# Optimization experiments

Measured on AMD Instinct MI355X. Metric: run time of the kernel, lower is better.

The kernel has to match this reference:

```python
import jax, jax.numpy as jnp
import numpy as np

N = 100000      # nodes
E = 1600000     # edges (avg degree 16)
F_IN = 128      # num_node_features (embedding vocab)
H = 32          # hidden_channels
C = 16          # num_classes
G = 64          # graphs in batch
NEG_SLOPE = 0.2  # GATConv default LeakyReLU slope


def setup_inputs() -> dict:
    key = jax.random.key(0)
    ks = jax.random.split(key, 12)
    x = jax.random.normal(ks[0], (N, F_IN), dtype=jnp.float32)
    edge_index = jax.random.randint(ks[1], (2, E), 0, N)
    batch = jnp.sort(jax.random.randint(ks[2], (N,), 0, G))
    s = 1.0 / np.sqrt(H).astype(np.float32)
    emb = jax.random.normal(ks[3], (F_IN, H), dtype=jnp.float32) * s
    W1 = jax.random.normal(ks[4], (H, H), dtype=jnp.float32) * s
    a1_src = jax.random.normal(ks[5], (H,), dtype=jnp.float32) * s
    a1_dst = jax.random.normal(ks[6], (H,), dtype=jnp.float32) * s
    b1 = jnp.zeros((H,), dtype=jnp.float32)
    W2 = jax.random.normal(ks[7], (H, C), dtype=jnp.float32) * s
    a2_src = jax.random.normal(ks[8], (C,), dtype=jnp.float32) * (1.0 / np.sqrt(C).astype(np.float32))
    a2_dst = jax.random.normal(ks[9], (C,), dtype=jnp.float32) * (1.0 / np.sqrt(C).astype(np.float32))
    b2 = jnp.zeros((C,), dtype=jnp.float32)
    return {"x": x, "edge_index": edge_index, "batch": batch,
            "emb": emb, "W1": W1, "a1_src": a1_src, "a1_dst": a1_dst, "b1": b1,
            "W2": W2, "a2_src": a2_src, "a2_dst": a2_dst, "b2": b2}


def gat_conv(h_in, src, dst, W, a_src, a_dst, bias):
    # h: [N, D]; per-edge attention alpha(e) = softmax_dst(leaky_relu(as[src]+ad[dst]))
    h = h_in @ W                                  # [N, D_out]
    al_s = h @ a_src                              # [N]
    al_d = h @ a_dst                              # [N]
    e = al_s[src] + al_d[dst]                     # [E]
    e = jnp.where(e > 0, e, NEG_SLOPE * e)        # leaky_relu
    m = jax.ops.segment_max(e, dst, num_segments=N)
    ex = jnp.exp(e - m[dst])
    denom = jax.ops.segment_sum(ex, dst, num_segments=N)
    alpha = ex / (denom[dst] + 1e-16)             # [E]
    out = jax.ops.segment_sum(alpha[:, None] * h[src], dst, num_segments=N)
    return out + bias


def reference(x, edge_index, batch, emb, W1, a1_src, a1_dst, b1, W2, a2_src, a2_dst, b2):
    # embedding lookup via argmax over feature dim
    idx = jnp.argmax(x, axis=1)                   # [N]
    h = emb[idx]                                  # [N, H]
    # add self loops (GATConv default)
    loops = jnp.arange(N, dtype=edge_index.dtype)
    src = jnp.concatenate([edge_index[0], loops])
    dst = jnp.concatenate([edge_index[1], loops])
    h = gat_conv(h, src, dst, W1, a1_src, a1_dst, b1)
    h = jax.nn.relu(h)
    # dropout is identity in eval mode
    h = gat_conv(h, src, dst, W2, a2_src, a2_dst, b2)   # [N, C]
    # global mean pool over graphs
    sums = jax.ops.segment_sum(h, batch, num_segments=G)         # [G, C]
    cnts = jax.ops.segment_sum(jnp.ones((N,), h.dtype), batch, num_segments=G)
    pooled = sums / jnp.maximum(cnts, 1.0)[:, None]
    return jax.nn.softmax(pooled, axis=1)
```

## Files before the change

kernel.cpp:

```cpp
#include <hip/hip_runtime.h>
#include <hip/hip_fp16.h>
#include <cmath>

#define HDIM 32
#define CDIM 16
#define FDIM 128
#define GDIM 64
#define NEG 0.2f
#define NN 100000
#define PPART 1024
#define CAPP 2048
#define WMAX 98
#define KA_BLOCKS 128

__device__ __forceinline__ float leaky(float e) { return e > 0.f ? e : NEG * e; }

__device__ __forceinline__ int part_of(int d) {
  return (int)(((unsigned)d << 10) / (unsigned)NN);
}
__device__ __forceinline__ int base_of(int p) {
  return (p * NN + (PPART - 1)) >> 10;
}

__global__ void k0_precompute(const float* __restrict__ emb, const float* __restrict__ W1,
                              const float* __restrict__ a1s, const float* __restrict__ a1d,
                              float* __restrict__ h1p, float* __restrict__ als1p,
                              float* __restrict__ ald1p) {
  __shared__ float sW1[HDIM * HDIM];
  int t = threadIdx.x;
  for (int i = t; i < HDIM * HDIM; i += 128) sW1[i] = W1[i];
  __syncthreads();
  int v = t;
  float hrow[HDIM];
#pragma unroll
  for (int k = 0; k < HDIM; ++k) hrow[k] = 0.f;
  for (int j = 0; j < HDIM; ++j) {
    float e = emb[v * HDIM + j];
#pragma unroll
    for (int k = 0; k < HDIM; ++k) hrow[k] += e * sW1[j * HDIM + k];
  }
  float s = 0.f, d = 0.f;
  for (int k = 0; k < HDIM; ++k) {
    h1p[v * HDIM + k] = hrow[k];
    s += hrow[k] * a1s[k];
    d += hrow[k] * a1d[k];
  }
  als1p[v] = s;
  ald1p[v] = d;
}

__global__ __launch_bounds__(256) void k1_argmax(const float* __restrict__ x,
                                                 int* __restrict__ idx, int N) {
  int wid = (blockIdx.x * blockDim.x + threadIdx.x) >> 6;
  int lane = threadIdx.x & 63;
  if (wid >= N) return;
  const float2* xr = (const float2*)(x + (size_t)wid * FDIM);
  float2 f = xr[lane];
  float best;
  int bi;
  if (f.y > f.x) { best = f.y; bi = 2 * lane + 1; } else { best = f.x; bi = 2 * lane; }
#pragma unroll
  for (int off = 32; off >= 1; off >>= 1) {
    float ov = __shfl_xor(best, off);
    int oi = __shfl_xor(bi, off);
    if (ov > best || (ov == best && oi < bi)) { best = ov; bi = oi; }
  }
  if (lane == 0) idx[wid] = bi;
}

__global__ __launch_bounds__(512) void kA_partition(const int* __restrict__ src,
                                                    const int* __restrict__ dst,
                                                    const int* __restrict__ idx,
                                                    int* __restrict__ pcnt,
                                                    unsigned* __restrict__ pay, int E) {
  __shared__ int lcount[PPART];
  __shared__ int gbase[PPART];
  int t = threadIdx.x;
  for (int i = t; i < PPART; i += 512) lcount[i] = 0;
  __syncthreads();
  int per = (E + KA_BLOCKS - 1) / KA_BLOCKS;
  int e0 = blockIdx.x * per, e1 = min(e0 + per, E);
  for (int e = e0 + t; e < e1; e += 512) atomicAdd(&lcount[part_of(dst[e])], 1);
  __syncthreads();
  for (int i = t; i < PPART; i += 512) gbase[i] = atomicAdd(&pcnt[i * 16], lcount[i]);
  __syncthreads();
  for (int e = e0 + t; e < e1; e += 512) {
    int d = dst[e], s = src[e];
    int p = part_of(d);
    int dloc = d - base_of(p);
    int pos = atomicAdd(&gbase[p], 1);
    if (pos < CAPP)
      pay[(size_t)p * CAPP + pos] =
          ((unsigned)dloc << 24) | ((unsigned)idx[s] << 17) | (unsigned)s;
  }
}

__global__ __launch_bounds__(512) void kB_layer1(const int* __restrict__ pcnt,
                                                 const unsigned* __restrict__ pay,
                                                 const int* __restrict__ idx,
                                                 const float* __restrict__ h1p,
                                                 const float* __restrict__ als1p,
                                                 const float* __restrict__ ald1p,
                                                 const float* __restrict__ b1,
                                                 const float* __restrict__ W2,
                                                 const float* __restrict__ a2s,
                                                 const float* __restrict__ a2d,
                                                 unsigned* __restrict__ pay2,
                                                 int* __restrict__ rpg,
                                                 __half2* __restrict__ h2h,
                                                 float* __restrict__ als2,
                                                 float* __restrict__ ald2, int N) {
  __shared__ float sh1p[FDIM * HDIM];
  __shared__ unsigned spay[CAPP];
  __shared__ int shist[WMAX];
  __shared__ int srp[WMAX + 1];
  __shared__ int soff[WMAX];
  __shared__ float sals1p[FDIM];
  __shared__ float sald1w[WMAX];
  __shared__ int sidxw[WMAX];
  __shared__ float sW2[HDIM * CDIM];
  __shared__ float sb1[HDIM];
  __shared__ float sa2s[CDIM], sa2d[CDIM];
  __shared__ float sstage[512];
  int t = threadIdx.x;
  int p = blockIdx.x;
  int base = base_of(p);
  int wend = base_of(p + 1); if (wend > N) wend = N;
  int wlen = wend - base;
  for (int i = t; i < FDIM * HDIM; i += 512) sh1p[i] = h1p[i];
  for (int i = t; i < HDIM * CDIM; i += 512) sW2[i] = W2[i];
  if (t < FDIM) sals1p[t] = als1p[t];
  if (t < HDIM) sb1[t] = b1[t];
  if (t < CDIM) { sa2s[t] = a2s[t]; sa2d[t] = a2d[t]; }
  if (t < WMAX) shist[t] = 0;
  for (int i = t; i < wlen; i += 512) {
    int ii = idx[base + i];
    sidxw[i] = ii;
    sald1w[i] = ald1p[ii];
  }
  __syncthreads();
  int cnt = min(pcnt[p * 16], CAPP);
  const unsigned* pm = pay + (size_t)p * CAPP;
  unsigned pwreg[4];
#pragma unroll
  for (int k = 0; k < 4; ++k) {
    int i = t + k * 512;
    if (i < cnt) {
      unsigned pw = pm[i];
      pwreg[k] = pw;
      atomicAdd(&shist[pw >> 24], 1);
    }
  }
  __syncthreads();
  if (t < 64) {
    int l = t;
    int v0 = (l < WMAX) ? shist[l] : 0;
    int v1 = (64 + l < WMAX) ? shist[64 + l] : 0;
    int s0 = v0, s1 = v1;
#pragma unroll
    for (int o = 1; o < 64; o <<= 1) {
      int u0 = __shfl_up(s0, o);
      int u1 = __shfl_up(s1, o);
      if (l >= o) { s0 += u0; s1 += u1; }
    }
    int tot0 = __shfl(s0, 63);
    if (l < WMAX) { srp[l] = s0 - v0; soff[l] = s0 - v0; }
    int i1 = 64 + l;
    if (i1 <= WMAX) {
      int ex = tot0 + s1 - v1;
      srp[i1] = ex;
      if (i1 < WMAX) soff[i1] = ex;
    }
  }
  __syncthreads();
#pragma unroll
  for (int k = 0; k < 4; ++k) {
    int i = t + k * 512;
    if (i < cnt) {
      unsigned pw = pwreg[k];
      int slot = atomicAdd(&soff[pw >> 24], 1);
      spay[slot] = pw;
    }
  }
  __syncthreads();
  for (int i = t; i < cnt; i += 512) pay2[(size_t)p * CAPP + i] = spay[i];
  for (int i = t; i <= wlen; i += 512) rpg[p * (WMAX + 1) + i] = srp[i];
  int g = t >> 5, c = t & 31;
  int j = c & 15, h = c >> 4;
  for (int i = g; i < wlen; i += 16) {
    int r0 = srp[i], r1 = srp[i + 1];
    float aldi = sald1w[i];
    float acc = 0.f, den = 0.f;
    for (int r = r0; r < r1; ++r) {
      unsigned pw = spay[r];
      int ivs = (pw >> 17) & 127;
      float w = __expf(leaky(sals1p[ivs] + aldi));
      acc += w * sh1p[ivs * HDIM + c];
      den += w;
    }
    int iv = sidxw[i];
    float wself = __expf(leaky(sals1p[iv] + aldi));
    acc += wself * sh1p[iv * HDIM + c];
    den += wself;
    float hr = fmaxf(acc / (den + 1e-16f) + sb1[c], 0.f);
    sstage[g * 32 + c] = hr;
    float pj = 0.f;
#pragma unroll
    for (int q = 0; q < 16; ++q) {
      int cc = h * 16 + q;
      pj += sstage[g * 32 + cc] * sW2[cc * CDIM + j];
    }
    pj += __shfl_xor(pj, 16);
    int n = base + i;
    float pjo = __shfl_xor(pj, 1);
    if (c < CDIM && !(c & 1))
      h2h[(size_t)n * 8 + (c >> 1)] = __floats2half2_rn(pj, pjo);
    float us = pj * sa2s[j], ud = pj * sa2d[j];
    us += __shfl_xor(us, 8); us += __shfl_xor(us, 4);
    us += __shfl_xor(us, 2); us += __shfl_xor(us, 1);
    ud += __shfl_xor(ud, 8); ud += __shfl_xor(ud, 4);
    ud += __shfl_xor(ud, 2); ud += __shfl_xor(ud, 1);
    if (c == 0) { als2[n] = us; ald2[n] = ud; }
  }
}

__global__ __launch_bounds__(512) void kC_layer2(const int* __restrict__ rpg,
                                                 const unsigned* __restrict__ pay2,
                                                 const float* __restrict__ als2,
                                                 const float* __restrict__ ald2,
                                                 const __half2* __restrict__ h2h,
                                                 const float* __restrict__ b2,
                                                 const int* __restrict__ batch,
                                                 float* __restrict__ pooled,
                                                 int* __restrict__ cnts, int N) {
  __shared__ int srp[WMAX + 1];
  __shared__ float sald2w[WMAX];
  __shared__ float sals2w[WMAX];
  __shared__ int sbatchw[WMAX];
  __shared__ float pl[GDIM * CDIM];
  __shared__ int cl[GDIM];
  __shared__ float sb2[CDIM];
  int t = threadIdx.x;
  int p = blockIdx.x;
  int base = base_of(p);
  int wend = base_of(p + 1); if (wend > N) wend = N;
  int wlen = wend - base;
  for (int i = t; i < GDIM * CDIM; i += 512) pl[i] = 0.f;
  if (t < GDIM) cl[t] = 0;
  if (t < CDIM) sb2[t] = b2[t];
  for (int i = t; i <= wlen; i += 512) srp[i] = rpg[p * (WMAX + 1) + i];
  for (int i = t; i < wlen; i += 512) {
    sald2w[i] = ald2[base + i];
    sals2w[i] = als2[base + i];
    sbatchw[i] = batch[base + i];
  }
  __syncthreads();
  const unsigned* pg = pay2 + (size_t)p * CAPP;
  int g = t >> 3, c2 = t & 7;
  for (int i = g; i < wlen; i += 64) {
    int r0 = srp[i], r1 = srp[i + 1];
    float aldi = sald2w[i];
    float accx = 0.f, accy = 0.f, den = 0.f;
    unsigned pw = (r0 < r1) ? pg[r0] : 0u;
    for (int r = r0; r < r1; ++r) {
      unsigned pwn = (r + 1 < r1) ? pg[r + 1] : 0u;
      int s = (int)(pw & 0x1FFFFu);
      float a = als2[s];
      float2 hf = __half22float2(h2h[(size_t)s * 8 + c2]);
      float w = __expf(leaky(a + aldi));
      accx += w * hf.x;
      accy += w * hf.y;
      den += w;
      pw = pwn;
    }
    int n = base + i;
    float wself = __expf(leaky(sals2w[i] + aldi));
    float2 hs = __half22float2(h2h[(size_t)n * 8 + c2]);
    accx += wself * hs.x;
    accy += wself * hs.y;
    den += wself;
    float inv = 1.f / (den + 1e-16f);
    float outx = accx * inv + sb2[2 * c2];
    float outy = accy * inv + sb2[2 * c2 + 1];
    int gg = sbatchw[i];
    atomicAdd(&pl[gg * CDIM + 2 * c2], outx);
    atomicAdd(&pl[gg * CDIM + 2 * c2 + 1], outy);
    if (c2 == 0) atomicAdd(&cl[gg], 1);
  }
  __syncthreads();
  for (int i = t; i < GDIM * CDIM; i += 512)
    if (pl[i] != 0.f) atomicAdd(&pooled[i], pl[i]);
  if (t < GDIM && cl[t]) atomicAdd(&cnts[t], cl[t]);
}

__global__ void k9_softmax(const float* __restrict__ pooled, const int* __restrict__ cnts,
                           float* __restrict__ out) {
  int g = threadIdx.x;
  if (g >= GDIM) return;
  float cnt = fmaxf((float)cnts[g], 1.f);
  float v[CDIM];
  float m = -1e30f;
  for (int j = 0; j < CDIM; ++j) {
    v[j] = pooled[g * CDIM + j] / cnt;
    m = fmaxf(m, v[j]);
  }
  float s = 0.f;
  for (int j = 0; j < CDIM; ++j) {
    v[j] = expf(v[j] - m);
    s += v[j];
  }
  for (int j = 0; j < CDIM; ++j) out[g * CDIM + j] = v[j] / s;
}

extern "C" void kernel_launch(void* const* d_in, const int* in_sizes, int n_in,
                              void* d_out, int out_size, void* d_ws, size_t ws_size,
                              hipStream_t stream) {
  const float* x = (const float*)d_in[0];
  const int* ei = (const int*)d_in[1];
  const int* batch = (const int*)d_in[2];
  const float* emb = (const float*)d_in[3];
  const float* W1 = (const float*)d_in[4];
  const float* a1s = (const float*)d_in[5];
  const float* a1d = (const float*)d_in[6];
  const float* b1 = (const float*)d_in[7];
  const float* W2 = (const float*)d_in[8];
  const float* a2s = (const float*)d_in[9];
  const float* a2d = (const float*)d_in[10];
  const float* b2 = (const float*)d_in[11];
  const int N = in_sizes[2];
  const int E = in_sizes[1] / 2;
  const int* src = ei;
  const int* dst = ei + E;

  float* w = (float*)d_ws;
  int* pcnt = (int*)w;  w += PPART * 16;
  float* pooled = w;    w += GDIM * CDIM;
  int* cnts = (int*)w;  w += GDIM;
  size_t zbytes = (size_t)((char*)w - (char*)d_ws);
  unsigned* pay = (unsigned*)w;  w += (size_t)PPART * CAPP;
  unsigned* pay2 = (unsigned*)w; w += (size_t)PPART * CAPP;
  int* rpg = (int*)w;            w += (size_t)PPART * (WMAX + 1);
  float* h1p = w;   w += FDIM * HDIM;
  float* als1p = w; w += FDIM;
  float* ald1p = w; w += FDIM;
  int* idx = (int*)w; w += N;
  __half2* h2h = (__half2*)w; w += (size_t)N * 8;
  float* als2 = w;  w += N;
  float* ald2 = w;  w += N;

  hipMemsetAsync(d_ws, 0, zbytes, stream);

  k0_precompute<<<1, 128, 0, stream>>>(emb, W1, a1s, a1d, h1p, als1p, ald1p);
  k1_argmax<<<(N + 3) / 4, 256, 0, stream>>>(x, idx, N);
  kA_partition<<<KA_BLOCKS, 512, 0, stream>>>(src, dst, idx, pcnt, pay, E);
  kB_layer1<<<PPART, 512, 0, stream>>>(pcnt, pay, idx, h1p, als1p, ald1p, b1, W2,
                                       a2s, a2d, pay2, rpg, h2h, als2, ald2, N);
  kC_layer2<<<PPART, 512, 0, stream>>>(rpg, pay2, als2, ald2, h2h, b2, batch,
                                       pooled, cnts, N);
  k9_softmax<<<1, 64, 0, stream>>>(pooled, cnts, (float*)d_out);
}
```

Measured before the change: 243.2 us.

## Partition edges into coarser regions and split each edge loop across two lanes

The edge partition now bins edges into 256 coarse destination regions instead of 1024 fine ones. It reuses per-thread slot counters in registers, so it no longer does a second atomic pass, and it no longer gathers idx in that kernel. The layer-1 kernel runs four blocks per region; each block scans the whole region payload, filters the edges for its quarter and gathers idx there. The layer-2 kernel splits each node's edge loop across two lane groups with software prefetch and combines them with a shuffle. The goal is less atomic contention and scattered-write cost in partitioning, and more memory-level parallelism in layer 2, at the price of each layer-1 block reading four times as much payload.

```diff
diff --git a/kernel.cpp b/kernel.cpp
--- a/kernel.cpp
+++ b/kernel.cpp
@@ -8,18 +8,21 @@
 #define GDIM 64
 #define NEG 0.2f
 #define NN 100000
+#define NREG 256
+#define CAPR 8192
+#define QS 98
 #define PPART 1024
 #define CAPP 2048
 #define WMAX 98
-#define KA_BLOCKS 128
+#define EPT 13
 
 __device__ __forceinline__ float leaky(float e) { return e > 0.f ? e : NEG * e; }
 
-__device__ __forceinline__ int part_of(int d) {
-  return (int)(((unsigned)d << 10) / (unsigned)NN);
-}
-__device__ __forceinline__ int base_of(int p) {
-  return (p * NN + (PPART - 1)) >> 10;
+__device__ __forceinline__ int reg_of(int d) {
+  return (int)(((unsigned)d << 8) / (unsigned)NN);
+}
+__device__ __forceinline__ int rbase_of(int r) {
+  return (r * NN + (NREG - 1)) >> 8;
 }
 
 __global__ void k0_precompute(const float* __restrict__ emb, const float* __restrict__ W1,
@@ -70,33 +73,47 @@
 
 __global__ __launch_bounds__(512) void kA_partition(const int* __restrict__ src,
                                                     const int* __restrict__ dst,
-                                                    const int* __restrict__ idx,
                                                     int* __restrict__ pcnt,
-                                                    unsigned* __restrict__ pay, int E) {
-  __shared__ int lcount[PPART];
-  __shared__ int gbase[PPART];
+                                                    unsigned* __restrict__ payR, int E) {
+  __shared__ int lcount[NREG];
+  __shared__ int gbase[NREG];
   int t = threadIdx.x;
-  for (int i = t; i < PPART; i += 512) lcount[i] = 0;
-  __syncthreads();
-  int per = (E + KA_BLOCKS - 1) / KA_BLOCKS;
+  if (t < NREG) lcount[t] = 0;
+  __syncthreads();
+  int per = (E + NREG - 1) / NREG;
   int e0 = blockIdx.x * per, e1 = min(e0 + per, E);
-  for (int e = e0 + t; e < e1; e += 512) atomicAdd(&lcount[part_of(dst[e])], 1);
-  __syncthreads();
-  for (int i = t; i < PPART; i += 512) gbase[i] = atomicAdd(&pcnt[i * 16], lcount[i]);
-  __syncthreads();
-  for (int e = e0 + t; e < e1; e += 512) {
-    int d = dst[e], s = src[e];
-    int p = part_of(d);
-    int dloc = d - base_of(p);
-    int pos = atomicAdd(&gbase[p], 1);
-    if (pos < CAPP)
-      pay[(size_t)p * CAPP + pos] =
-          ((unsigned)dloc << 24) | ((unsigned)idx[s] << 17) | (unsigned)s;
+  int dreg[EPT], slotg[EPT];
+#pragma unroll
+  for (int k = 0; k < EPT; ++k) {
+    int e = e0 + t + k * 512;
+    if (e < e1) {
+      int d = dst[e];
+      dreg[k] = d;
+      slotg[k] = atomicAdd(&lcount[reg_of(d)], 1);
+    }
+  }
+  __syncthreads();
+  if (t < NREG) gbase[t] = atomicAdd(&pcnt[t * 16], lcount[t]);
+  __syncthreads();
+#pragma unroll
+  for (int k = 0; k < EPT; ++k) {
+    int e = e0 + t + k * 512;
+    if (e < e1) {
+      int d = dreg[k], s = src[e];
+      int r = reg_of(d);
+      int dloc = d - rbase_of(r);
+      int q = dloc / QS;
+      int loc = dloc - q * QS;
+      int pos = gbase[r] + slotg[k];
+      if (pos < CAPR)
+        payR[(size_t)r * CAPR + pos] =
+            ((unsigned)q << 30) | ((unsigned)loc << 17) | (unsigned)s;
+    }
   }
 }
 
 __global__ __launch_bounds__(512) void kB_layer1(const int* __restrict__ pcnt,
-                                                 const unsigned* __restrict__ pay,
+                                                 const unsigned* __restrict__ payR,
                                                  const int* __restrict__ idx,
                                                  const float* __restrict__ h1p,
                                                  const float* __restrict__ als1p,
@@ -124,9 +141,12 @@
   __shared__ float sstage[512];
   int t = threadIdx.x;
   int p = blockIdx.x;
-  int base = base_of(p);
-  int wend = base_of(p + 1); if (wend > N) wend = N;
-  int wlen = wend - base;
+  int r = p >> 2, q = p & 3;
+  int rbase = rbase_of(r);
+  int rend = rbase_of(r + 1); if (rend > N) rend = N;
+  int nbase = rbase + q * QS;
+  int nend = min(nbase + QS, rend);
+  int wlen = nend - nbase;
   for (int i = t; i < FDIM * HDIM; i += 512) sh1p[i] = h1p[i];
   for (int i = t; i < HDIM * CDIM; i += 512) sW2[i] = W2[i];
   if (t < FDIM) sals1p[t] = als1p[t];
@@ -134,22 +154,16 @@
   if (t < CDIM) { sa2s[t] = a2s[t]; sa2d[t] = a2d[t]; }
   if (t < WMAX) shist[t] = 0;
   for (int i = t; i < wlen; i += 512) {
-    int ii = idx[base + i];
+    int ii = idx[nbase + i];
     sidxw[i] = ii;
     sald1w[i] = ald1p[ii];
   }
   __syncthreads();
-  int cnt = min(pcnt[p * 16], CAPP);
-  const unsigned* pm = pay + (size_t)p * CAPP;
-  unsigned pwreg[4];
-#pragma unroll
-  for (int k = 0; k < 4; ++k) {
-    int i = t + k * 512;
-    if (i < cnt) {
-      unsigned pw = pm[i];
-      pwreg[k] = pw;
-      atomicAdd(&shist[pw >> 24], 1);
-    }
+  int cntR = min(pcnt[r * 16], CAPR);
+  const unsigned* pm = payR + (size_t)r * CAPR;
+  for (int i = t; i < cntR; i += 512) {
+    unsigned pw = pm[i];
+    if ((int)(pw >> 30) == q) atomicAdd(&shist[(pw >> 17) & 127], 1);
   }
   __syncthreads();
   if (t < 64) {
@@ -173,26 +187,29 @@
     }
   }
   __syncthreads();
-#pragma unroll
-  for (int k = 0; k < 4; ++k) {
-    int i = t + k * 512;
-    if (i < cnt) {
-      unsigned pw = pwreg[k];
-      int slot = atomicAdd(&soff[pw >> 24], 1);
-      spay[slot] = pw;
-    }
-  }
-  __syncthreads();
-  for (int i = t; i < cnt; i += 512) pay2[(size_t)p * CAPP + i] = spay[i];
+  for (int i = t; i < cntR; i += 512) {
+    unsigned pw = pm[i];
+    if ((int)(pw >> 30) == q) {
+      int loc = (pw >> 17) & 127;
+      int s = (int)(pw & 0x1FFFFu);
+      int iv = idx[s];
+      int slot = atomicAdd(&soff[loc], 1);
+      if (slot < CAPP)
+        spay[slot] = ((unsigned)loc << 24) | ((unsigned)iv << 17) | (unsigned)s;
+    }
+  }
+  __syncthreads();
+  int kept = min(srp[WMAX], CAPP);
+  for (int i = t; i < kept; i += 512) pay2[(size_t)p * CAPP + i] = spay[i];
   for (int i = t; i <= wlen; i += 512) rpg[p * (WMAX + 1) + i] = srp[i];
   int g = t >> 5, c = t & 31;
   int j = c & 15, h = c >> 4;
   for (int i = g; i < wlen; i += 16) {
-    int r0 = srp[i], r1 = srp[i + 1];
+    int r0 = srp[i], r1 = min(srp[i + 1], CAPP);
     float aldi = sald1w[i];
     float acc = 0.f, den = 0.f;
-    for (int r = r0; r < r1; ++r) {
-      unsigned pw = spay[r];
+    for (int e = r0; e < r1; ++e) {
+      unsigned pw = spay[e];
       int ivs = (pw >> 17) & 127;
       float w = __expf(leaky(sals1p[ivs] + aldi));
       acc += w * sh1p[ivs * HDIM + c];
@@ -206,12 +223,12 @@
     sstage[g * 32 + c] = hr;
     float pj = 0.f;
 #pragma unroll
-    for (int q = 0; q < 16; ++q) {
-      int cc = h * 16 + q;
+    for (int qq = 0; qq < 16; ++qq) {
+      int cc = h * 16 + qq;
       pj += sstage[g * 32 + cc] * sW2[cc * CDIM + j];
     }
     pj += __shfl_xor(pj, 16);
-    int n = base + i;
+    int n = nbase + i;
     float pjo = __shfl_xor(pj, 1);
     if (c < CDIM && !(c & 1))
       h2h[(size_t)n * 8 + (c >> 1)] = __floats2half2_rn(pj, pjo);
@@ -242,50 +259,74 @@
   __shared__ float sb2[CDIM];
   int t = threadIdx.x;
   int p = blockIdx.x;
-  int base = base_of(p);
-  int wend = base_of(p + 1); if (wend > N) wend = N;
-  int wlen = wend - base;
+  int r = p >> 2, q = p & 3;
+  int rbase = rbase_of(r);
+  int rend = rbase_of(r + 1); if (rend > N) rend = N;
+  int nbase = rbase + q * QS;
+  int nend = min(nbase + QS, rend);
+  int wlen = nend - nbase;
   for (int i = t; i < GDIM * CDIM; i += 512) pl[i] = 0.f;
   if (t < GDIM) cl[t] = 0;
   if (t < CDIM) sb2[t] = b2[t];
   for (int i = t; i <= wlen; i += 512) srp[i] = rpg[p * (WMAX + 1) + i];
   for (int i = t; i < wlen; i += 512) {
-    sald2w[i] = ald2[base + i];
-    sals2w[i] = als2[base + i];
-    sbatchw[i] = batch[base + i];
+    sald2w[i] = ald2[nbase + i];
+    sals2w[i] = als2[nbase + i];
+    sbatchw[i] = batch[nbase + i];
   }
   __syncthreads();
   const unsigned* pg = pay2 + (size_t)p * CAPP;
-  int g = t >> 3, c2 = t & 7;
-  for (int i = g; i < wlen; i += 64) {
-    int r0 = srp[i], r1 = srp[i + 1];
+  int g = t >> 4;
+  int c2 = t & 7;
+  int ep = (t >> 3) & 1;
+  for (int i = g; i < wlen; i += 32) {
+    int r0 = srp[i], r1 = min(srp[i + 1], CAPP);
     float aldi = sald2w[i];
     float accx = 0.f, accy = 0.f, den = 0.f;
-    unsigned pw = (r0 < r1) ? pg[r0] : 0u;
-    for (int r = r0; r < r1; ++r) {
-      unsigned pwn = (r + 1 < r1) ? pg[r + 1] : 0u;
-      int s = (int)(pw & 0x1FFFFu);
-      float a = als2[s];
-      float2 hf = __half22float2(h2h[(size_t)s * 8 + c2]);
-      float w = __expf(leaky(a + aldi));
-      accx += w * hf.x;
-      accy += w * hf.y;
+    int e = r0 + ep;
+    float a_cur = 0.f;
+    float2 h_cur = make_float2(0.f, 0.f);
+    if (e < r1) {
+      int s = (int)(pg[e] & 0x1FFFFu);
+      a_cur = als2[s];
+      h_cur = __half22float2(h2h[(size_t)s * 8 + c2]);
+    }
+    for (; e < r1; e += 2) {
+      int en = e + 2;
+      float a_n = 0.f;
+      float2 h_n = make_float2(0.f, 0.f);
+      bool has_n = en < r1;
+      if (has_n) {
+        int sn = (int)(pg[en] & 0x1FFFFu);
+        a_n = als2[sn];
+        h_n = __half22float2(h2h[(size_t)sn * 8 + c2]);
+      }
+      float w = __expf(leaky(a_cur + aldi));
+      accx += w * h_cur.x;
+      accy += w * h_cur.y;
       den += w;
-      pw = pwn;
-    }
-    int n = base + i;
-    float wself = __expf(leaky(sals2w[i] + aldi));
-    float2 hs = __half22float2(h2h[(size_t)n * 8 + c2]);
-    accx += wself * hs.x;
-    accy += wself * hs.y;
-    den += wself;
-    float inv = 1.f / (den + 1e-16f);
-    float outx = accx * inv + sb2[2 * c2];
-    float outy = accy * inv + sb2[2 * c2 + 1];
-    int gg = sbatchw[i];
-    atomicAdd(&pl[gg * CDIM + 2 * c2], outx);
-    atomicAdd(&pl[gg * CDIM + 2 * c2 + 1], outy);
-    if (c2 == 0) atomicAdd(&cl[gg], 1);
+      a_cur = a_n;
+      h_cur = h_n;
+      if (!has_n) break;
+    }
+    accx += __shfl_xor(accx, 8);
+    accy += __shfl_xor(accy, 8);
+    den += __shfl_xor(den, 8);
+    if (ep == 0) {
+      int n = nbase + i;
+      float wself = __expf(leaky(sals2w[i] + aldi));
+      float2 hs = __half22float2(h2h[(size_t)n * 8 + c2]);
+      accx += wself * hs.x;
+      accy += wself * hs.y;
+      den += wself;
+      float inv = 1.f / (den + 1e-16f);
+      float outx = accx * inv + sb2[2 * c2];
+      float outy = accy * inv + sb2[2 * c2 + 1];
+      int gg = sbatchw[i];
+      atomicAdd(&pl[gg * CDIM + 2 * c2], outx);
+      atomicAdd(&pl[gg * CDIM + 2 * c2 + 1], outy);
+      if (c2 == 0) atomicAdd(&cl[gg], 1);
+    }
   }
   __syncthreads();
   for (int i = t; i < GDIM * CDIM; i += 512)
@@ -333,11 +374,11 @@
   const int* dst = ei + E;
 
   float* w = (float*)d_ws;
-  int* pcnt = (int*)w;  w += PPART * 16;
+  int* pcnt = (int*)w;  w += NREG * 16;
   float* pooled = w;    w += GDIM * CDIM;
   int* cnts = (int*)w;  w += GDIM;
   size_t zbytes = (size_t)((char*)w - (char*)d_ws);
-  unsigned* pay = (unsigned*)w;  w += (size_t)PPART * CAPP;
+  unsigned* payR = (unsigned*)w; w += (size_t)NREG * CAPR;
   unsigned* pay2 = (unsigned*)w; w += (size_t)PPART * CAPP;
   int* rpg = (int*)w;            w += (size_t)PPART * (WMAX + 1);
   float* h1p = w;   w += FDIM * HDIM;
@@ -352,8 +393,8 @@
 
   k0_precompute<<<1, 128, 0, stream>>>(emb, W1, a1s, a1d, h1p, als1p, ald1p);
   k1_argmax<<<(N + 3) / 4, 256, 0, stream>>>(x, idx, N);
-  kA_partition<<<KA_BLOCKS, 512, 0, stream>>>(src, dst, idx, pcnt, pay, E);
-  kB_layer1<<<PPART, 512, 0, stream>>>(pcnt, pay, idx, h1p, als1p, ald1p, b1, W2,
+  kA_partition<<<NREG, 512, 0, stream>>>(src, dst, pcnt, payR, E);
+  kB_layer1<<<PPART, 512, 0, stream>>>(pcnt, payR, idx, h1p, als1p, ald1p, b1, W2,
                                        a2s, a2d, pay2, rpg, h2h, als2, ald2, N);
   kC_layer2<<<PPART, 512, 0, stream>>>(rpg, pay2, als2, ald2, h2h, b2, batch,
                                        pooled, cnts, N);
```

Result: no change. 244.8 us (+0.7%).
